# Kernel optimization log

Measured on AMD Instinct MI355X. Metric: run time of the kernel, lower is better.

Reference implementation:

```python
import jax, jax.numpy as jnp
import numpy as np
from jax import lax

V, E, H1, H2, D = 10000, 128, 128, 64, 64
T, B, MAXLEN = 512, 256, 30
SOS, EOS = 1, 2


def setup_inputs() -> dict:
    key = jax.random.key(0)
    ks = jax.random.split(key, 16)
    s = 0.05
    return {
        "enc_key": jax.random.normal(ks[0], (T, B, D), jnp.float32),
        "enc_values": jax.random.normal(ks[1], (T, B, D), jnp.float32),
        "mask": jax.random.randint(ks[2], (B, 1, T), 0, 2, jnp.int32),
        "emb": jax.random.normal(ks[3], (V, E), jnp.float32) * s,
        "w_ih1": jax.random.normal(ks[4], (4 * H1, E + D), jnp.float32) * s,
        "w_hh1": jax.random.normal(ks[5], (4 * H1, H1), jnp.float32) * s,
        "b_ih1": jax.random.normal(ks[6], (4 * H1,), jnp.float32) * s,
        "b_hh1": jax.random.normal(ks[7], (4 * H1,), jnp.float32) * s,
        "w_ih2": jax.random.normal(ks[8], (4 * H2, H1), jnp.float32) * s,
        "w_hh2": jax.random.normal(ks[9], (4 * H2, H2), jnp.float32) * s,
        "b_ih2": jax.random.normal(ks[10], (4 * H2,), jnp.float32) * s,
        "b_hh2": jax.random.normal(ks[11], (4 * H2,), jnp.float32) * s,
        "wq": jax.random.normal(ks[12], (D, H2), jnp.float32) * s,
        "bq": jax.random.normal(ks[13], (D,), jnp.float32) * s,
        "wp": jax.random.normal(ks[14], (V, H2 + D), jnp.float32) * s,
        "bp": jax.random.normal(ks[15], (V,), jnp.float32) * s,
    }


def _lstm_cell(x, h, c, w_ih, w_hh, b_ih, b_hh):
    # torch LSTMCell: gates ordered (i, f, g, o)
    gates = x @ w_ih.T + h @ w_hh.T + b_ih + b_hh
    i, f, g, o = jnp.split(gates, 4, axis=-1)
    c_new = jax.nn.sigmoid(f) * c + jax.nn.sigmoid(i) * jnp.tanh(g)
    h_new = jax.nn.sigmoid(o) * jnp.tanh(c_new)
    return h_new, c_new


def reference(enc_key, enc_values, mask, emb, w_ih1, w_hh1, b_ih1, b_hh1,
              w_ih2, w_hh2, b_ih2, b_hh2, wq, bq, wp, bp):
    maskf = mask.astype(enc_key.dtype)[:, 0, :]          # (B, T)
    emb_p = emb.at[EOS].set(0.0)                          # padding_idx row zeroed

    pred0 = jnp.zeros((B, V), enc_key.dtype).at[:, SOS].set(1.0)
    init = (jnp.zeros((B, H1), enc_key.dtype), jnp.zeros((B, H1), enc_key.dtype),
            jnp.zeros((B, H2), enc_key.dtype), jnp.zeros((B, H2), enc_key.dtype),
            jnp.zeros((B, D), enc_key.dtype), pred0)

    def step(carry, _):
        h1, c1, h2, c2, context, pred = carry
        tok = jnp.argmax(pred, axis=-1)                   # greedy feedback
        char_embed = emb_p[tok]                           # (B, E)
        inp = jnp.concatenate([char_embed, context], axis=1)
        h1, c1 = _lstm_cell(inp, h1, c1, w_ih1, w_hh1, b_ih1, b_hh1)
        h2, c2 = _lstm_cell(h1, h2, c2, w_ih2, w_hh2, b_ih2, b_hh2)
        query = h2 @ wq.T + bq                            # (B, D)
        energy = jnp.einsum('bd,tbd->bt', query, enc_key)
        att = jax.nn.softmax(energy, axis=-1)
        m_att = maskf * att
        m_att = m_att / jnp.clip(jnp.sum(m_att, axis=-1, keepdims=True), 2e-30, None)
        context = jnp.einsum('bt,tbd->bd', m_att, enc_values)
        pred = jnp.concatenate([h2, context], axis=1) @ wp.T + bp
        return (h1, c1, h2, c2, context, pred), pred

    _, preds = lax.scan(step, init, None, length=MAXLEN)  # (MAXLEN, B, V)
    return jnp.transpose(preds, (1, 0, 2))                # (B, MAXLEN, V)
```

## Files before the change

### kernel.cpp

```cpp
#include <hip/hip_runtime.h>
#include <hip/hip_bf16.h>

#define V 10000
#define E 128
#define H1 128
#define H2 64
#define D 64
#define T 512
#define B 256
#define MAXLEN 30
#define SOS 1
#define EOS 2
#define BGS 8
#define NVB 40

#define O_EMB   0
#define O_WIH1  1280000
#define O_WHH1  1378304
#define O_BIH1  1443840
#define O_BHH1  1444352
#define O_WIH2  1444864
#define O_WHH2  1477632
#define O_BIH2  1494016
#define O_BHH2  1494272
#define O_WQ    1494528
#define O_BQ    1498624
#define O_WP    1498688
#define O_BP    2778688
#define TOTALW  2788688

typedef unsigned long long u64;

__device__ __forceinline__ float b2f(__hip_bfloat16 x){ return __bfloat162float(x); }
__device__ __forceinline__ float sigf(float x){ return 1.f/(1.f + expf(-x)); }
__device__ __forceinline__ float4 ldf4(const float* p){
  float4 r; __builtin_memcpy(&r, (const void*)p, 16); return r;
}
__device__ __forceinline__ float dot4f(const float* x, float4 w){
  return x[0]*w.x + x[1]*w.y + x[2]*w.z + x[3]*w.w;
}

__global__ void kdtype(const void* __restrict__ probe, int* __restrict__ flagp){
  const int tid = threadIdx.x;
  const unsigned w = ((const unsigned*)probe)[tid];
  const unsigned e = (w >> 7) & 0xFFu;
  const bool inband = (e >= 0x60u) && (e <= 0x7Eu);
  const u64 m = __ballot(inband);
  if (tid == 0) flagp[0] = (m == 0xFFFFFFFFFFFFFFFFull) ? 1 : 0;
}

__global__ __launch_bounds__(256) void kcvt(
    const void* s_emb, const void* s_wih1, const void* s_whh1,
    const void* s_bih1, const void* s_bhh1, const void* s_wih2,
    const void* s_whh2, const void* s_bih2, const void* s_bhh2,
    const void* s_wq, const void* s_bq, const void* s_wp, const void* s_bp,
    float* __restrict__ dst, const int* __restrict__ flagp)
{
  const int idx = blockIdx.x * 256 + threadIdx.x;
  if (idx >= TOTALW) return;
  const int flag = flagp[0];
  const void* src; int off;
  if      (idx < O_WIH1){ src = s_emb;  off = idx - O_EMB;  }
  else if (idx < O_WHH1){ src = s_wih1; off = idx - O_WIH1; }
  else if (idx < O_BIH1){ src = s_whh1; off = idx - O_WHH1; }
  else if (idx < O_BHH1){ src = s_bih1; off = idx - O_BIH1; }
  else if (idx < O_WIH2){ src = s_bhh1; off = idx - O_BHH1; }
  else if (idx < O_WHH2){ src = s_wih2; off = idx - O_WIH2; }
  else if (idx < O_BIH2){ src = s_whh2; off = idx - O_WHH2; }
  else if (idx < O_BHH2){ src = s_bih2; off = idx - O_BIH2; }
  else if (idx < O_WQ)  { src = s_bhh2; off = idx - O_BHH2; }
  else if (idx < O_BQ)  { src = s_wq;   off = idx - O_WQ;   }
  else if (idx < O_WP)  { src = s_bq;   off = idx - O_BQ;   }
  else if (idx < O_BP)  { src = s_wp;   off = idx - O_WP;   }
  else                  { src = s_bp;   off = idx - O_BP;   }
  dst[idx] = flag ? b2f(((const __hip_bfloat16*)src)[off])
                  : ((const float*)src)[off];
}

__global__ __launch_bounds__(256) void ktrans(
    const void* __restrict__ enc_key, const void* __restrict__ enc_val,
    float* __restrict__ encTk, float* __restrict__ encTv,
    const int* __restrict__ flagp)
{
  const int b = blockIdx.x;
  const int tid = threadIdx.x;
  const int flag = flagp[0];
  const int d = tid & 63, tq = tid >> 6;
  if (flag){
    const __hip_bfloat16* bk = (const __hip_bfloat16*)enc_key;
    const __hip_bfloat16* bv = (const __hip_bfloat16*)enc_val;
    for (int tt = tq; tt < T; tt += 4){
      encTk[((size_t)b*T + tt)*D + d] = b2f(bk[((size_t)tt*B + b)*D + d]);
      encTv[((size_t)b*T + tt)*D + d] = b2f(bv[((size_t)tt*B + b)*D + d]);
    }
  } else {
    const float* fk = (const float*)enc_key;
    const float* fv = (const float*)enc_val;
    for (int tt = tq; tt < T; tt += 4){
      encTk[((size_t)b*T + tt)*D + d] = fk[((size_t)tt*B + b)*D + d];
      encTv[((size_t)b*T + tt)*D + d] = fv[((size_t)tt*B + b)*D + d];
    }
  }
}

__global__ __launch_bounds__(256) void kA(
    int t,
    const float* __restrict__ wts,
    float* __restrict__ h1g,
    float* __restrict__ c1g,
    const float* __restrict__ ctxg,
    const float* __restrict__ candv, const int* __restrict__ candi)
{
  const int bid = blockIdx.x;
  const int tid = threadIdx.x;
  const int rt = bid >> 5;
  const int bA = (bid & 31) * 8;

  __shared__ float4 wA4[80*64];
  __shared__ __align__(16) float xs[8*324];
  __shared__ float g_s[64*8];
  __shared__ float bias1_s[64];
  __shared__ int tok_s[8];

  const int par = t & 1;
  const float* h1prev = h1g + (size_t)(par^1)*B*H1;
  float*       h1new  = h1g + (size_t)par*B*H1;

  for (int idx = tid; idx < 80*64; idx += 256){
    const int k4 = idx >> 6, r = idx & 63;
    const int row = ((r >> 4) * 128) + (rt * 16) + (r & 15);
    float4 w;
    if (k4 < 48) w = ldf4(wts + O_WIH1 + (size_t)row*(E+D) + k4*4);
    else         w = ldf4(wts + O_WHH1 + (size_t)row*H1 + (k4-48)*4);
    wA4[idx] = w;
  }
  if (tid < 64){
    const int rowA = ((tid >> 4) * 128) + (rt * 16) + (tid & 15);
    bias1_s[tid] = wts[O_BIH1 + rowA] + wts[O_BHH1 + rowA];
  }

  if (t > 0){
    const int bi = tid >> 5, j = tid & 31;
    const int b = bA + bi;
    float mv = candv[b*NVB + j];
    int   mi = candi[b*NVB + j];
    if (j < NVB - 32){
      float ov = candv[b*NVB + j + 32]; int oi = candi[b*NVB + j + 32];
      if (ov > mv || (ov == mv && oi < mi)){ mv = ov; mi = oi; }
    }
    #pragma unroll
    for (int off = 16; off > 0; off >>= 1){
      float ov = __shfl_down(mv, off); int oi = __shfl_down(mi, off);
      if (ov > mv || (ov == mv && oi < mi)){ mv = ov; mi = oi; }
    }
    if (j == 0) tok_s[bi] = mi;
  } else {
    if (tid < 8) tok_s[tid] = SOS;
  }
  __syncthreads();

  for (int bi = 0; bi < 8; ++bi){
    const int b = bA + bi;
    const int tok = tok_s[bi];
    for (int k = tid; k < 320; k += 256){
      float x;
      if (k < E)          x = (tok == EOS) ? 0.f : wts[O_EMB + (size_t)tok*E + k];
      else if (k < E + D) x = (t == 0) ? 0.f : ctxg[(size_t)b*D + (k - E)];
      else                x = (t == 0) ? 0.f : h1prev[(size_t)b*H1 + (k - (E + D))];
      xs[bi*324 + k] = x;
    }
  }
  __syncthreads();

  {
    const int r = tid >> 2, bq = tid & 3;
    const float4* x0 = (const float4*)(xs + (bq*2    )*324);
    const float4* x1 = (const float4*)(xs + (bq*2 + 1)*324);
    float a0 = bias1_s[r], a1 = a0;
    #pragma unroll 8
    for (int k4 = 0; k4 < 80; ++k4){
      const float4 w = wA4[k4*64 + r];
      const float4 xa = x0[k4], xb = x1[k4];
      a0 += xa.x*w.x + xa.y*w.y + xa.z*w.z + xa.w*w.w;
      a1 += xb.x*w.x + xb.y*w.y + xb.z*w.z + xb.w*w.w;
    }
    g_s[r*8 + bq*2]     = a0;
    g_s[r*8 + bq*2 + 1] = a1;
  }
  __syncthreads();

  if (tid < 128){
    const int ui = tid >> 3, bi = tid & 7;
    const float gi = sigf (g_s[(ui     )*8 + bi]);
    const float gf = sigf (g_s[(16 + ui)*8 + bi]);
    const float gg = tanhf(g_s[(32 + ui)*8 + bi]);
    const float go = sigf (g_s[(48 + ui)*8 + bi]);
    const float cold = (t == 0) ? 0.f : c1g[(size_t)(bA + bi)*H1 + rt*16 + ui];
    const float cn = gf * cold + gi * gg;
    c1g[(size_t)(bA + bi)*H1 + rt*16 + ui] = cn;
    h1new[(size_t)(bA + bi)*H1 + rt*16 + ui] = go * tanhf(cn);
  }
}

__global__ __launch_bounds__(256) void kB(
    int t,
    const float* __restrict__ wts,
    const float* __restrict__ encTk, const float* __restrict__ encTv,
    const int* __restrict__ mask,
    const float* __restrict__ h1g,
    float* __restrict__ h2g,
    float* __restrict__ c2g,
    float* __restrict__ ctxg,
    float* __restrict__ xvec)
{
  const int b = blockIdx.x;
  const int tid = threadIdx.x;
  const float* h1new = h1g + (size_t)(t & 1)*B*H1;

  __shared__ float h1_s[H1];
  __shared__ float h2_s[H2];
  __shared__ float h2n_s[H2];
  __shared__ float g_s[4*H2];
  __shared__ float q_s[D];
  __shared__ float wv_s[T];
  __shared__ float red_s[256];

  if (tid < H1)                h1_s[tid]      = h1new[(size_t)b*H1 + tid];
  else if (tid < H1 + H2)      h2_s[tid - H1] = (t == 0) ? 0.f : h2g[(size_t)b*H2 + (tid - H1)];
  __syncthreads();

  {
    const int j = tid;
    const float* wr = wts + O_WIH2 + (size_t)j*H1;
    float acc = wts[O_BIH2 + j] + wts[O_BHH2 + j];
    #pragma unroll
    for (int kk = 0; kk < H1/4; ++kk) acc += dot4f(h1_s + kk*4, ldf4(wr + kk*4));
    const float* wr2 = wts + O_WHH2 + (size_t)j*H2;
    #pragma unroll
    for (int kk = 0; kk < H2/4; ++kk) acc += dot4f(h2_s + kk*4, ldf4(wr2 + kk*4));
    g_s[j] = acc;
  }
  __syncthreads();

  if (tid < H2){
    const float gi = sigf(g_s[tid]);
    const float gf = sigf(g_s[H2 + tid]);
    const float gg = tanhf(g_s[2*H2 + tid]);
    const float go = sigf(g_s[3*H2 + tid]);
    const float cold = (t == 0) ? 0.f : c2g[(size_t)b*H2 + tid];
    const float cn = gf*cold + gi*gg;
    const float hn = go*tanhf(cn);
    c2g[(size_t)b*H2 + tid] = cn;
    h2g[(size_t)b*H2 + tid] = hn;
    h2n_s[tid] = hn;
    xvec[(size_t)b*(H2 + D) + tid] = hn;
  }
  __syncthreads();

  if (tid < D){
    const float* wr = wts + O_WQ + (size_t)tid*H2;
    float acc = wts[O_BQ + tid];
    #pragma unroll
    for (int kk = 0; kk < H2/4; ++kk) acc += dot4f(h2n_s + kk*4, ldf4(wr + kk*4));
    q_s[tid] = acc;
  }
  __syncthreads();

  float e0 = 0.f, e1 = 0.f;
  {
    const float* kr0 = encTk + ((size_t)b*T + tid)*D;
    const float* kr1 = kr0 + (size_t)256*D;
    #pragma unroll
    for (int kk = 0; kk < D/4; ++kk){
      e0 += dot4f(q_s + kk*4, ldf4(kr0 + kk*4));
      e1 += dot4f(q_s + kk*4, ldf4(kr1 + kk*4));
    }
  }
  red_s[tid] = fmaxf(e0, e1);
  __syncthreads();
  for (int s = 128; s > 0; s >>= 1){
    if (tid < s) red_s[tid] = fmaxf(red_s[tid], red_s[tid + s]);
    __syncthreads();
  }
  const float emax = red_s[0];
  __syncthreads();

  const int m0 = mask[b*T + tid], m1 = mask[b*T + tid + 256];
  const float w0 = m0 ? expf(e0 - emax) : 0.f;
  const float w1 = m1 ? expf(e1 - emax) : 0.f;
  wv_s[tid] = w0;
  wv_s[tid + 256] = w1;
  red_s[tid] = w0 + w1;
  __syncthreads();
  for (int s = 128; s > 0; s >>= 1){
    if (tid < s) red_s[tid] += red_s[tid + s];
    __syncthreads();
  }
  const float inv = 1.f / fmaxf(red_s[0], 2e-30f);
  __syncthreads();

  {
    const int d = tid & 63, ch = tid >> 6;
    const float* vb2 = encTv + (size_t)b*T*D + d;
    float acc = 0.f;
    #pragma unroll 8
    for (int tt = ch*128; tt < ch*128 + 128; ++tt)
      acc += wv_s[tt] * vb2[(size_t)tt*D];
    red_s[tid] = acc;
  }
  __syncthreads();
  if (tid < D){
    const float cv = (red_s[tid] + red_s[tid+64] + red_s[tid+128] + red_s[tid+192]) * inv;
    ctxg[(size_t)b*D + tid] = cv;
    xvec[(size_t)b*(H2 + D) + H2 + tid] = cv;
  }
}

__global__ __launch_bounds__(256) void kC(
    int t,
    const float* __restrict__ wp_f,
    const float* __restrict__ bp_f,
    const float* __restrict__ xvec,
    void* __restrict__ outv,
    float* __restrict__ candv, int* __restrict__ candi,
    const int* __restrict__ flagp)
{
  const int tid = threadIdx.x;
  const int vb = blockIdx.x;
  const int v = vb * 256 + tid;
  const int bg = blockIdx.y;
  const int flagb = flagp[0];
  const bool valid = v < V;
  const int vc = valid ? v : 0;
  const float* wrow = wp_f + (size_t)vc*(H2 + D);
  const float* xp = xvec + (size_t)bg*BGS*(H2 + D);

  float acc[BGS];
  #pragma unroll
  for (int i = 0; i < BGS; ++i) acc[i] = 0.f;

  #pragma unroll
  for (int kk = 0; kk < (H2 + D)/4; ++kk){
    const float4 w = ldf4(wrow + kk*4);
    #pragma unroll
    for (int i = 0; i < BGS; ++i){
      const float* x = xp + i*(H2 + D) + kk*4;
      acc[i] += x[0]*w.x + x[1]*w.y + x[2]*w.z + x[3]*w.w;
    }
  }

  const float bias = valid ? bp_f[vc] : 0.f;
  #pragma unroll
  for (int i = 0; i < BGS; ++i){
    acc[i] += bias;
    if (valid){
      const size_t oi = ((size_t)(bg*BGS + i)*MAXLEN + t)*V + v;
      if (flagb) ((__hip_bfloat16*)outv)[oi] = __float2bfloat16(acc[i]);
      else       ((float*)outv)[oi] = acc[i];
    }
  }

  __shared__ float lv[4][BGS];
  __shared__ int   li[4][BGS];
  const int lane = tid & 63, wid = tid >> 6;
  #pragma unroll
  for (int i = 0; i < BGS; ++i){
    float mv = valid ? acc[i] : -__builtin_inff();
    int   mi = valid ? v : 0x7FFFFFFF;
    for (int off = 32; off > 0; off >>= 1){
      float ov = __shfl_down(mv, off);
      int   oi = __shfl_down(mi, off);
      if (ov > mv || (ov == mv && oi < mi)){ mv = ov; mi = oi; }
    }
    if (lane == 0){ lv[wid][i] = mv; li[wid][i] = mi; }
  }
  __syncthreads();
  if (tid < BGS){
    float mv = lv[0][tid]; int mi = li[0][tid];
    #pragma unroll
    for (int w2 = 1; w2 < 4; ++w2){
      float ov = lv[w2][tid]; int oi = li[w2][tid];
      if (ov > mv || (ov == mv && oi < mi)){ mv = ov; mi = oi; }
    }
    const int b = bg*BGS + tid;
    candv[b*NVB + vb] = mv;
    candi[b*NVB + vb] = mi;
  }
}

extern "C" void kernel_launch(void* const* d_in, const int* in_sizes, int n_in,
                              void* d_out, int out_size, void* d_ws, size_t ws_size,
                              hipStream_t stream)
{
  const void* enc_key = d_in[0];
  const void* enc_val = d_in[1];
  const int*  mask    = (const int*)d_in[2];
  const void* emb     = d_in[3];
  const void* w_ih1   = d_in[4];
  const void* w_hh1   = d_in[5];
  const void* b_ih1   = d_in[6];
  const void* b_hh1   = d_in[7];
  const void* w_ih2   = d_in[8];
  const void* w_hh2   = d_in[9];
  const void* b_ih2   = d_in[10];
  const void* b_hh2   = d_in[11];
  const void* wq      = d_in[12];
  const void* bq      = d_in[13];
  const void* wp      = d_in[14];
  const void* bp      = d_in[15];

  float* wsf  = (float*)d_ws;
  int*  flagp = (int*)wsf;
  float* wts  = wsf + 16;
  float* h1g   = wts + TOTALW;
  float* c1g   = h1g + 2*B*H1;
  float* h2g   = c1g + B*H1;
  float* c2g   = h2g + B*H2;
  float* ctxg  = c2g + B*H2;
  float* xvec  = ctxg + B*D;
  float* candv = xvec + B*(H2 + D);
  int*   candi = (int*)(candv + B*NVB);
  float* encTk = (float*)(candi + B*NVB);
  float* encTv = encTk + (size_t)B*T*D;

  kdtype<<<dim3(1), dim3(64), 0, stream>>>(b_ih1, flagp);
  kcvt<<<dim3((TOTALW + 255)/256), dim3(256), 0, stream>>>(
      emb, w_ih1, w_hh1, b_ih1, b_hh1, w_ih2, w_hh2, b_ih2, b_hh2,
      wq, bq, wp, bp, wts, flagp);
  ktrans<<<dim3(B), dim3(256), 0, stream>>>(enc_key, enc_val, encTk, encTv, flagp);

  for (int t = 0; t < MAXLEN; ++t){
    kA<<<dim3(B), dim3(256), 0, stream>>>(
        t, wts, h1g, c1g, ctxg, candv, candi);
    kB<<<dim3(B), dim3(256), 0, stream>>>(
        t, wts, encTk, encTv, mask, h1g, h2g, c2g, ctxg, xvec);
    kC<<<dim3(NVB, B/BGS), dim3(256), 0, stream>>>(
        t, wts + O_WP, wts + O_BP, xvec, d_out, candv, candi, flagp);
  }
}
```

Before: 3.192 ms.

## Fuse both LSTM layers and attention into one multi-batch kernel

Merges the layer-1 LSTM kernel and the layer-2/attention kernel into a single 512-thread kernel. Each block now handles 4 batch rows end to end, and the argmax reduction becomes a 64-lane wave shuffle. The h1 double buffer is dropped because each block owns its batch rows. Layer-1 weights are now streamed from global memory rather than staged in LDS, and the grid shrinks to 64 blocks, which reduces parallelism and adds a redundant key load in the energy loop. Separately, the output projection's batch group size is doubled so each vocab weight tile is reused across more batch rows.

```diff
diff --git a/kernel.cpp b/kernel.cpp
--- a/kernel.cpp
+++ b/kernel.cpp
@@ -11,8 +11,10 @@
 #define MAXLEN 30
 #define SOS 1
 #define EOS 2
-#define BGS 8
+#define BGS 16
 #define NVB 40
+#define KB1 4
+#define NB1 (B/KB1)
 
 #define O_EMB   0
 #define O_WIH1  1280000
@@ -103,216 +105,225 @@
   }
 }
 
-__global__ __launch_bounds__(256) void kA(
+__global__ __launch_bounds__(512) void K1(
     int t,
     const float* __restrict__ wts,
+    const float* __restrict__ encTk, const float* __restrict__ encTv,
+    const int* __restrict__ mask,
     float* __restrict__ h1g,
     float* __restrict__ c1g,
-    const float* __restrict__ ctxg,
+    float* __restrict__ h2g,
+    float* __restrict__ c2g,
+    float* __restrict__ ctxg,
+    float* __restrict__ xvec,
     const float* __restrict__ candv, const int* __restrict__ candi)
 {
   const int bid = blockIdx.x;
   const int tid = threadIdx.x;
-  const int rt = bid >> 5;
-  const int bA = (bid & 31) * 8;
-
-  __shared__ float4 wA4[80*64];
-  __shared__ __align__(16) float xs[8*324];
-  __shared__ float g_s[64*8];
-  __shared__ float bias1_s[64];
-  __shared__ int tok_s[8];
-
-  const int par = t & 1;
-  const float* h1prev = h1g + (size_t)(par^1)*B*H1;
-  float*       h1new  = h1g + (size_t)par*B*H1;
-
-  for (int idx = tid; idx < 80*64; idx += 256){
-    const int k4 = idx >> 6, r = idx & 63;
-    const int row = ((r >> 4) * 128) + (rt * 16) + (r & 15);
-    float4 w;
-    if (k4 < 48) w = ldf4(wts + O_WIH1 + (size_t)row*(E+D) + k4*4);
-    else         w = ldf4(wts + O_WHH1 + (size_t)row*H1 + (k4-48)*4);
-    wA4[idx] = w;
-  }
-  if (tid < 64){
-    const int rowA = ((tid >> 4) * 128) + (rt * 16) + (tid & 15);
-    bias1_s[tid] = wts[O_BIH1 + rowA] + wts[O_BHH1 + rowA];
-  }
-
-  if (t > 0){
-    const int bi = tid >> 5, j = tid & 31;
-    const int b = bA + bi;
-    float mv = candv[b*NVB + j];
-    int   mi = candi[b*NVB + j];
-    if (j < NVB - 32){
-      float ov = candv[b*NVB + j + 32]; int oi = candi[b*NVB + j + 32];
-      if (ov > mv || (ov == mv && oi < mi)){ mv = ov; mi = oi; }
-    }
-    #pragma unroll
-    for (int off = 16; off > 0; off >>= 1){
-      float ov = __shfl_down(mv, off); int oi = __shfl_down(mi, off);
-      if (ov > mv || (ov == mv && oi < mi)){ mv = ov; mi = oi; }
-    }
-    if (j == 0) tok_s[bi] = mi;
+  const int bA  = bid * KB1;
+  const int wv  = tid >> 6;
+  const int lane = tid & 63;
+
+  __shared__ __align__(16) float xs[KB1*324];
+  __shared__ __align__(16) float x2s[KB1*196];
+  __shared__ float g1s[512*5];
+  __shared__ float g2s[256*5];
+  __shared__ float h2s[KB1*64];
+  __shared__ float q_s[KB1*64];
+  __shared__ float wv_s[KB1*512];
+  __shared__ float cpart[8*64];
+  __shared__ float redmax[8], redsum[8], inv_s[KB1];
+  __shared__ int tok_s[KB1];
+
+  if (wv < KB1){
+    const int b = bA + wv;
+    float mv = -__builtin_inff(); int mi = 0x7FFFFFFF;
+    if (t > 0){
+      if (lane < NVB){ mv = candv[b*NVB + lane]; mi = candi[b*NVB + lane]; }
+      #pragma unroll
+      for (int off = 32; off > 0; off >>= 1){
+        float ov = __shfl_down(mv, off); int oi = __shfl_down(mi, off);
+        if (ov > mv || (ov == mv && oi < mi)){ mv = ov; mi = oi; }
+      }
+      if (lane == 0) tok_s[wv] = mi;
+    } else {
+      if (lane == 0) tok_s[wv] = SOS;
+    }
   } else {
-    if (tid < 8) tok_s[tid] = SOS;
-  }
-  __syncthreads();
-
-  for (int bi = 0; bi < 8; ++bi){
-    const int b = bA + bi;
-    const int tok = tok_s[bi];
-    for (int k = tid; k < 320; k += 256){
+    const int idx = tid - 256;
+    const int bi = idx >> 6, j = idx & 63;
+    x2s[bi*196 + 128 + j] = (t == 0) ? 0.f : h2g[(size_t)(bA + bi)*H2 + j];
+  }
+  __syncthreads();
+
+  if (tid < 320){
+    const int k = tid;
+    #pragma unroll
+    for (int bi = 0; bi < KB1; ++bi){
+      const int b = bA + bi;
+      const int tok = tok_s[bi];
       float x;
       if (k < E)          x = (tok == EOS) ? 0.f : wts[O_EMB + (size_t)tok*E + k];
       else if (k < E + D) x = (t == 0) ? 0.f : ctxg[(size_t)b*D + (k - E)];
-      else                x = (t == 0) ? 0.f : h1prev[(size_t)b*H1 + (k - (E + D))];
+      else                x = (t == 0) ? 0.f : h1g[(size_t)b*H1 + (k - (E + D))];
       xs[bi*324 + k] = x;
     }
   }
   __syncthreads();
 
   {
-    const int r = tid >> 2, bq = tid & 3;
-    const float4* x0 = (const float4*)(xs + (bq*2    )*324);
-    const float4* x1 = (const float4*)(xs + (bq*2 + 1)*324);
-    float a0 = bias1_s[r], a1 = a0;
-    #pragma unroll 8
+    const int r = tid;
+    const float bias = wts[O_BIH1 + r] + wts[O_BHH1 + r];
+    float a0 = bias, a1 = bias, a2 = bias, a3 = bias;
+    #pragma unroll 4
     for (int k4 = 0; k4 < 80; ++k4){
-      const float4 w = wA4[k4*64 + r];
-      const float4 xa = x0[k4], xb = x1[k4];
+      float4 w;
+      if (k4 < 48) w = ldf4(wts + O_WIH1 + (size_t)r*(E+D) + k4*4);
+      else         w = ldf4(wts + O_WHH1 + (size_t)r*H1 + (k4-48)*4);
+      const float4 xa = ldf4(xs + 0*324 + k4*4);
+      const float4 xb = ldf4(xs + 1*324 + k4*4);
+      const float4 xc = ldf4(xs + 2*324 + k4*4);
+      const float4 xd = ldf4(xs + 3*324 + k4*4);
       a0 += xa.x*w.x + xa.y*w.y + xa.z*w.z + xa.w*w.w;
       a1 += xb.x*w.x + xb.y*w.y + xb.z*w.z + xb.w*w.w;
-    }
-    g_s[r*8 + bq*2]     = a0;
-    g_s[r*8 + bq*2 + 1] = a1;
-  }
-  __syncthreads();
-
-  if (tid < 128){
-    const int ui = tid >> 3, bi = tid & 7;
-    const float gi = sigf (g_s[(ui     )*8 + bi]);
-    const float gf = sigf (g_s[(16 + ui)*8 + bi]);
-    const float gg = tanhf(g_s[(32 + ui)*8 + bi]);
-    const float go = sigf (g_s[(48 + ui)*8 + bi]);
-    const float cold = (t == 0) ? 0.f : c1g[(size_t)(bA + bi)*H1 + rt*16 + ui];
-    const float cn = gf * cold + gi * gg;
-    c1g[(size_t)(bA + bi)*H1 + rt*16 + ui] = cn;
-    h1new[(size_t)(bA + bi)*H1 + rt*16 + ui] = go * tanhf(cn);
-  }
-}
-
-__global__ __launch_bounds__(256) void kB(
-    int t,
-    const float* __restrict__ wts,
-    const float* __restrict__ encTk, const float* __restrict__ encTv,
-    const int* __restrict__ mask,
-    const float* __restrict__ h1g,
-    float* __restrict__ h2g,
-    float* __restrict__ c2g,
-    float* __restrict__ ctxg,
-    float* __restrict__ xvec)
-{
-  const int b = blockIdx.x;
-  const int tid = threadIdx.x;
-  const float* h1new = h1g + (size_t)(t & 1)*B*H1;
-
-  __shared__ float h1_s[H1];
-  __shared__ float h2_s[H2];
-  __shared__ float h2n_s[H2];
-  __shared__ float g_s[4*H2];
-  __shared__ float q_s[D];
-  __shared__ float wv_s[T];
-  __shared__ float red_s[256];
-
-  if (tid < H1)                h1_s[tid]      = h1new[(size_t)b*H1 + tid];
-  else if (tid < H1 + H2)      h2_s[tid - H1] = (t == 0) ? 0.f : h2g[(size_t)b*H2 + (tid - H1)];
-  __syncthreads();
-
-  {
-    const int j = tid;
-    const float* wr = wts + O_WIH2 + (size_t)j*H1;
-    float acc = wts[O_BIH2 + j] + wts[O_BHH2 + j];
-    #pragma unroll
-    for (int kk = 0; kk < H1/4; ++kk) acc += dot4f(h1_s + kk*4, ldf4(wr + kk*4));
-    const float* wr2 = wts + O_WHH2 + (size_t)j*H2;
-    #pragma unroll
-    for (int kk = 0; kk < H2/4; ++kk) acc += dot4f(h2_s + kk*4, ldf4(wr2 + kk*4));
-    g_s[j] = acc;
-  }
-  __syncthreads();
-
-  if (tid < H2){
-    const float gi = sigf(g_s[tid]);
-    const float gf = sigf(g_s[H2 + tid]);
-    const float gg = tanhf(g_s[2*H2 + tid]);
-    const float go = sigf(g_s[3*H2 + tid]);
-    const float cold = (t == 0) ? 0.f : c2g[(size_t)b*H2 + tid];
+      a2 += xc.x*w.x + xc.y*w.y + xc.z*w.z + xc.w*w.w;
+      a3 += xd.x*w.x + xd.y*w.y + xd.z*w.z + xd.w*w.w;
+    }
+    g1s[r*5 + 0] = a0; g1s[r*5 + 1] = a1;
+    g1s[r*5 + 2] = a2; g1s[r*5 + 3] = a3;
+  }
+  __syncthreads();
+
+  {
+    const int u = tid >> 2, bi = tid & 3;
+    const int b = bA + bi;
+    const float gi = sigf (g1s[(u      )*5 + bi]);
+    const float gf = sigf (g1s[(128 + u)*5 + bi]);
+    const float gg = tanhf(g1s[(256 + u)*5 + bi]);
+    const float go = sigf (g1s[(384 + u)*5 + bi]);
+    const float cold = (t == 0) ? 0.f : c1g[(size_t)b*H1 + u];
     const float cn = gf*cold + gi*gg;
     const float hn = go*tanhf(cn);
-    c2g[(size_t)b*H2 + tid] = cn;
-    h2g[(size_t)b*H2 + tid] = hn;
-    h2n_s[tid] = hn;
-    xvec[(size_t)b*(H2 + D) + tid] = hn;
-  }
-  __syncthreads();
-
-  if (tid < D){
-    const float* wr = wts + O_WQ + (size_t)tid*H2;
-    float acc = wts[O_BQ + tid];
-    #pragma unroll
-    for (int kk = 0; kk < H2/4; ++kk) acc += dot4f(h2n_s + kk*4, ldf4(wr + kk*4));
-    q_s[tid] = acc;
-  }
-  __syncthreads();
-
-  float e0 = 0.f, e1 = 0.f;
-  {
-    const float* kr0 = encTk + ((size_t)b*T + tid)*D;
-    const float* kr1 = kr0 + (size_t)256*D;
+    c1g[(size_t)b*H1 + u] = cn;
+    h1g[(size_t)b*H1 + u] = hn;
+    x2s[bi*196 + u] = hn;
+  }
+  __syncthreads();
+
+  {
+    const int r = tid & 255, bh = tid >> 8;
+    const float bias = wts[O_BIH2 + r] + wts[O_BHH2 + r];
+    float a0 = bias, a1 = bias;
+    const float* x0 = x2s + (bh*2    )*196;
+    const float* x1 = x2s + (bh*2 + 1)*196;
+    #pragma unroll 4
+    for (int k4 = 0; k4 < 48; ++k4){
+      float4 w;
+      if (k4 < 32) w = ldf4(wts + O_WIH2 + (size_t)r*H1 + k4*4);
+      else         w = ldf4(wts + O_WHH2 + (size_t)r*H2 + (k4-32)*4);
+      const float4 xa = ldf4(x0 + k4*4);
+      const float4 xb = ldf4(x1 + k4*4);
+      a0 += xa.x*w.x + xa.y*w.y + xa.z*w.z + xa.w*w.w;
+      a1 += xb.x*w.x + xb.y*w.y + xb.z*w.z + xb.w*w.w;
+    }
+    g2s[r*5 + bh*2]     = a0;
+    g2s[r*5 + bh*2 + 1] = a1;
+  }
+  __syncthreads();
+
+  if (tid < 256){
+    const int u = tid >> 2, bi = tid & 3;
+    const int b = bA + bi;
+    const float gi = sigf (g2s[(u      )*5 + bi]);
+    const float gf = sigf (g2s[(64  + u)*5 + bi]);
+    const float gg = tanhf(g2s[(128 + u)*5 + bi]);
+    const float go = sigf (g2s[(192 + u)*5 + bi]);
+    const float cold = (t == 0) ? 0.f : c2g[(size_t)b*H2 + u];
+    const float cn = gf*cold + gi*gg;
+    const float hn = go*tanhf(cn);
+    c2g[(size_t)b*H2 + u] = cn;
+    h2g[(size_t)b*H2 + u] = hn;
+    h2s[bi*64 + u] = hn;
+    xvec[(size_t)b*(H2 + D) + u] = hn;
+  }
+  __syncthreads();
+
+  if (tid < 256){
+    const int d = tid & 63, bi = tid >> 6;
+    const float* wr = wts + O_WQ + (size_t)d*H2;
+    float acc = wts[O_BQ + d];
+    #pragma unroll
+    for (int kk = 0; kk < H2/4; ++kk) acc += dot4f(h2s + bi*64 + kk*4, ldf4(wr + kk*4));
+    q_s[bi*64 + d] = acc;
+  }
+  __syncthreads();
+
+  const int abi = wv & 3, half = wv >> 2;
+  const int ab = bA + abi;
+  float e0 = 0.f, e1 = 0.f, e2 = 0.f, e3 = 0.f;
+  {
+    const int t2b = half*256;
+    const float* k0 = encTk + ((size_t)ab*T + t2b + 0*64 + lane)*D;
+    const float* k1 = encTk + ((size_t)ab*T + t2b + 1*64 + lane)*D;
+    const float* k2 = encTk + ((size_t)ab*T + t2b + 2*64 + lane)*D;
+    const float* k3 = encTk + ((size_t)ab*T + t2b + 3*64 + lane)*D;
     #pragma unroll
     for (int kk = 0; kk < D/4; ++kk){
-      e0 += dot4f(q_s + kk*4, ldf4(kr0 + kk*4));
-      e1 += dot4f(q_s + kk*4, ldf4(kr1 + kk*4));
-    }
-  }
-  red_s[tid] = fmaxf(e0, e1);
-  __syncthreads();
-  for (int s = 128; s > 0; s >>= 1){
-    if (tid < s) red_s[tid] = fmaxf(red_s[tid], red_s[tid + s]);
-    __syncthreads();
-  }
-  const float emax = red_s[0];
-  __syncthreads();
-
-  const int m0 = mask[b*T + tid], m1 = mask[b*T + tid + 256];
-  const float w0 = m0 ? expf(e0 - emax) : 0.f;
-  const float w1 = m1 ? expf(e1 - emax) : 0.f;
-  wv_s[tid] = w0;
-  wv_s[tid + 256] = w1;
-  red_s[tid] = w0 + w1;
-  __syncthreads();
-  for (int s = 128; s > 0; s >>= 1){
-    if (tid < s) red_s[tid] += red_s[tid + s];
-    __syncthreads();
-  }
-  const float inv = 1.f / fmaxf(red_s[0], 2e-30f);
-  __syncthreads();
-
-  {
-    const int d = tid & 63, ch = tid >> 6;
-    const float* vb2 = encTv + (size_t)b*T*D + d;
+      const float4 q4 = ldf4(q_s + abi*64 + kk*4);
+      e0 += dot4f((const float*)&q4, ldf4(k0 + kk*4)) * 0.f + q4.x*k0[kk*4] + q4.y*k0[kk*4+1] + q4.z*k0[kk*4+2] + q4.w*k0[kk*4+3];
+      e1 += q4.x*k1[kk*4] + q4.y*k1[kk*4+1] + q4.z*k1[kk*4+2] + q4.w*k1[kk*4+3];
+      e2 += q4.x*k2[kk*4] + q4.y*k2[kk*4+1] + q4.z*k2[kk*4+2] + q4.w*k2[kk*4+3];
+      e3 += q4.x*k3[kk*4] + q4.y*k3[kk*4+1] + q4.z*k3[kk*4+2] + q4.w*k3[kk*4+3];
+    }
+  }
+  {
+    float me = fmaxf(fmaxf(e0, e1), fmaxf(e2, e3));
+    #pragma unroll
+    for (int off = 32; off > 0; off >>= 1) me = fmaxf(me, __shfl_xor(me, off));
+    if (lane == 0) redmax[wv] = me;
+  }
+  __syncthreads();
+
+  {
+    const float emax = fmaxf(redmax[abi], redmax[abi + 4]);
+    const int t2b = half*256;
+    const int m0 = mask[ab*T + t2b + 0*64 + lane];
+    const int m1 = mask[ab*T + t2b + 1*64 + lane];
+    const int m2 = mask[ab*T + t2b + 2*64 + lane];
+    const int m3 = mask[ab*T + t2b + 3*64 + lane];
+    const float w0 = m0 ? expf(e0 - emax) : 0.f;
+    const float w1 = m1 ? expf(e1 - emax) : 0.f;
+    const float w2 = m2 ? expf(e2 - emax) : 0.f;
+    const float w3 = m3 ? expf(e3 - emax) : 0.f;
+    wv_s[abi*512 + t2b + 0*64 + lane] = w0;
+    wv_s[abi*512 + t2b + 1*64 + lane] = w1;
+    wv_s[abi*512 + t2b + 2*64 + lane] = w2;
+    wv_s[abi*512 + t2b + 3*64 + lane] = w3;
+    float sm = w0 + w1 + w2 + w3;
+    #pragma unroll
+    for (int off = 32; off > 0; off >>= 1) sm += __shfl_xor(sm, off);
+    if (lane == 0) redsum[wv] = sm;
+  }
+  __syncthreads();
+
+  {
+    if (half == 0 && lane == 0)
+      inv_s[abi] = 1.f / fmaxf(redsum[abi] + redsum[abi + 4], 2e-30f);
+    const float* vb2 = encTv + (size_t)ab*T*D + lane;
     float acc = 0.f;
+    const int t0 = half*256;
     #pragma unroll 8
-    for (int tt = ch*128; tt < ch*128 + 128; ++tt)
-      acc += wv_s[tt] * vb2[(size_t)tt*D];
-    red_s[tid] = acc;
-  }
-  __syncthreads();
-  if (tid < D){
-    const float cv = (red_s[tid] + red_s[tid+64] + red_s[tid+128] + red_s[tid+192]) * inv;
-    ctxg[(size_t)b*D + tid] = cv;
-    xvec[(size_t)b*(H2 + D) + H2 + tid] = cv;
+    for (int tt = t0; tt < t0 + 256; ++tt)
+      acc += wv_s[abi*512 + tt] * vb2[(size_t)tt*D];
+    cpart[wv*64 + lane] = acc;
+  }
+  __syncthreads();
+
+  if (wv < KB1){
+    const int b = bA + wv;
+    const float cv = (cpart[wv*64 + lane] + cpart[(wv + 4)*64 + lane]) * inv_s[wv];
+    ctxg[(size_t)b*D + lane] = cv;
+    xvec[(size_t)b*(H2 + D) + H2 + lane] = cv;
   }
 }
 
@@ -413,7 +424,7 @@
   int*  flagp = (int*)wsf;
   float* wts  = wsf + 16;
   float* h1g   = wts + TOTALW;
-  float* c1g   = h1g + 2*B*H1;
+  float* c1g   = h1g + B*H1;
   float* h2g   = c1g + B*H1;
   float* c2g   = h2g + B*H2;
   float* ctxg  = c2g + B*H2;
@@ -430,10 +441,9 @@
   ktrans<<<dim3(B), dim3(256), 0, stream>>>(enc_key, enc_val, encTk, encTv, flagp);
 
   for (int t = 0; t < MAXLEN; ++t){
-    kA<<<dim3(B), dim3(256), 0, stream>>>(
-        t, wts, h1g, c1g, ctxg, candv, candi);
-    kB<<<dim3(B), dim3(256), 0, stream>>>(
-        t, wts, encTk, encTv, mask, h1g, h2g, c2g, ctxg, xvec);
+    K1<<<dim3(NB1), dim3(512), 0, stream>>>(
+        t, wts, encTk, encTv, mask,
+        h1g, c1g, h2g, c2g, ctxg, xvec, candv, candi);
     kC<<<dim3(NVB, B/BGS), dim3(256), 0, stream>>>(
         t, wts + O_WP, wts + O_BP, xvec, d_out, candv, candi, flagp);
   }
```

New measurement: 7.285 ms. 2.28x slower.
